# Kernel optimization log

Measured on AMD Instinct MI355X. Metric: run time of the kernel, lower is better.

The kernel has to match this reference:

```python
import jax, jax.numpy as jnp
import numpy as np

B, T, IN, D = 32, 1024, 1536, 768


def setup_inputs() -> dict:
    key = jax.random.key(0)
    ks = jax.random.split(key, 14)
    s_in = 1.0 / np.sqrt(IN)
    s_d = 1.0 / np.sqrt(D)
    return {
        "x": jax.random.normal(ks[0], (B, T, IN), jnp.float32),
        # fc1/fc2 torch Linear weights stored [out, in]
        "fc1_w": jax.random.normal(ks[1], (IN, IN), jnp.float32) * s_in,
        "fc1_b": jax.random.normal(ks[2], (IN,), jnp.float32) * 0.01,
        "fc2_w": jax.random.normal(ks[3], (D, IN), jnp.float32) * s_in,
        "fc2_b": jax.random.normal(ks[4], (D,), jnp.float32) * 0.01,
        # Unary: Conv1d(D,D,k=1) then Conv1d(D,1,k=1); k=1 conv == per-token linear
        "un_emb_w": jax.random.normal(ks[5], (D, D), jnp.float32) * s_d,
        "un_emb_b": jax.random.normal(ks[6], (D,), jnp.float32) * 0.01,
        "un_red_w": jax.random.normal(ks[7], (1, D), jnp.float32) * s_d,
        "un_red_b": jax.random.normal(ks[8], (1,), jnp.float32) * 0.01,
        # Self Pairwise: x_embedding / y_embedding Conv1d(D,D,k=1)
        "pw_x_w": jax.random.normal(ks[9], (D, D), jnp.float32) * s_d,
        "pw_x_b": jax.random.normal(ks[10], (D,), jnp.float32) * 0.01,
        "pw_y_w": jax.random.normal(ks[11], (D, D), jnp.float32) * s_d,
        "pw_y_b": jax.random.normal(ks[12], (D,), jnp.float32) * 0.01,
        # reduce_potentials: Conv1d(2,1,k=1,bias=False) -> 2 scalars
        "red_w": jax.random.normal(ks[13], (2,), jnp.float32),
    }


def reference(x, fc1_w, fc1_b, fc2_w, fc2_b,
              un_emb_w, un_emb_b, un_red_w, un_red_b,
              pw_x_w, pw_x_b, pw_y_w, pw_y_b, red_w):
    # FGAEmbedder MLP: fc2(relu(fc1(x)))
    h = jax.nn.relu(jnp.einsum('bti,oi->bto', x, fc1_w) + fc1_b)
    u = jnp.einsum('bti,oi->bto', h, fc2_w) + fc2_b            # [B,T,D]

    # Unary potential (dropout is identity at inference)
    e = jax.nn.relu(jnp.einsum('btd,od->bto', u, un_emb_w) + un_emb_b)
    un_pot = (jnp.einsum('btd,od->bto', e, un_red_w) + un_red_b)[..., 0]  # [B,T]

    # Self pairwise: cosine-similarity matrix, marginalized by mean (spatial_dim=None)
    xe = jnp.einsum('btd,od->bto', u, pw_x_w) + pw_x_b
    ye = jnp.einsum('btd,od->bto', u, pw_y_w) + pw_y_b
    xn = xe / jnp.maximum(jnp.linalg.norm(xe, axis=-1, keepdims=True), 1e-12)
    yn = ye / jnp.maximum(jnp.linalg.norm(ye, axis=-1, keepdims=True), 1e-12)
    S = jnp.einsum('btd,bsd->bts', xn, yn)                     # [B,T,T]
    pw_pot = jnp.mean(S, axis=2)                               # [B,T]

    # reduce potentials (Conv1d 2->1 no bias; order: unary then self), softmax attention
    scores = red_w[0] * un_pot + red_w[1] * pw_pot             # [B,T]
    w = jax.nn.softmax(scores, axis=1)
    return jnp.einsum('btd,bt->bd', u, w)                      # [B,D]
```

## Files before the change

kernel.cpp:

```cpp
#include <hip/hip_runtime.h>
#include <stdint.h>

#define MROWS 32768
#define TSEQ  1024
#define BBATCH 32
#define INDIM 1536
#define DDIM  768
#define NCAT  2304

typedef short short8 __attribute__((ext_vector_type(8)));
typedef short short4v __attribute__((ext_vector_type(4)));
typedef float f32x4  __attribute__((ext_vector_type(4)));

__device__ __forceinline__ float b2f(ushort u) {
    union { uint32_t u; float f; } x; x.u = ((uint32_t)u) << 16; return x.f;
}
__device__ __forceinline__ ushort f2b(float f) {
    union { float f; uint32_t u; } x; x.f = f;
    uint32_t r = x.u + 0x7fffu + ((x.u >> 16) & 1u);
    return (ushort)(r >> 16);
}

__global__ void cvt_bf16(const float* __restrict__ in, ushort* __restrict__ out, int n4) {
    int i = blockIdx.x * blockDim.x + threadIdx.x;
    if (i < n4) {
        float4 v = ((const float4*)in)[i];
        ushort4 o;
        o.x = f2b(v.x); o.y = f2b(v.y); o.z = f2b(v.z); o.w = f2b(v.w);
        ((ushort4*)out)[i] = o;
    }
}

__device__ __forceinline__ void cvt4(const float* __restrict__ in, ushort* __restrict__ out, int i) {
    float4 v = ((const float4*)in)[i];
    ushort4 o;
    o.x = f2b(v.x); o.y = f2b(v.y); o.z = f2b(v.z); o.w = f2b(v.w);
    ((ushort4*)out)[i] = o;
}

__global__ void cvt_weights(const float* __restrict__ fc1_w, const float* __restrict__ fc2_w,
                            const float* __restrict__ w3a, const float* __restrict__ w3b,
                            const float* __restrict__ w3c,
                            const float* __restrict__ ba, const float* __restrict__ bb,
                            const float* __restrict__ bc,
                            ushort* __restrict__ W1, ushort* __restrict__ W2,
                            ushort* __restrict__ W3, float* __restrict__ B3,
                            float* __restrict__ ybar_zero, float* __restrict__ out_zero)
{
    int i = blockIdx.x * 256 + threadIdx.x;
    if (i < 589824)        cvt4(fc1_w, W1, i);
    else if (i < 884736)   cvt4(fc2_w, W2, i - 589824);
    else if (i < 1032192)  cvt4(w3a,  W3,           i - 884736);
    else if (i < 1179648)  cvt4(w3b,  W3 + 589824,  i - 1032192);
    else if (i < 1327104)  cvt4(w3c,  W3 + 1179648, i - 1179648);
    else if (i < 1327680) {
        int j = i - 1327104;
        const float* src = (j < 192) ? ba : (j < 384) ? bb : bc;
        int off = (j < 192) ? j : (j < 384) ? (j - 192) : (j - 384);
        ((float4*)B3)[j] = ((const float4*)src)[off];
    }
    else if (i < 1333824) {
        float4 z = {0.f, 0.f, 0.f, 0.f};
        ((float4*)ybar_zero)[i - 1327680] = z;
    }
    else if (i < 1339968) {
        float4 z = {0.f, 0.f, 0.f, 0.f};
        ((float4*)out_zero)[i - 1333824] = z;
    }
}

__global__ __launch_bounds__(256, 2)
void gemm_bt(const ushort* __restrict__ A, const ushort* __restrict__ Bm,
             const float* __restrict__ bias, ushort* __restrict__ C,
             int M, int N, int K, int relu_ncols)
{
    __shared__ __align__(16) ushort lA[128 * 64];
    __shared__ __align__(16) ushort lB[128 * 64];

    const int tid  = threadIdx.x;
    const int lane = tid & 63, wave = tid >> 6;
    const int wm = wave & 1, wn = wave >> 1;
    const int quad = lane >> 4, r16 = lane & 15;

    const int ntiles = N >> 7;
    const int xcd = blockIdx.x & 7;
    const int j   = blockIdx.x >> 3;
    const int g   = j / ntiles;
    const int n_t = j - g * ntiles;
    const int m_t = xcd + (g << 3);
    const int m0 = m_t * 128, n0 = n_t * 128;

    const int srow = lane >> 2;
    const int scol = ((lane & 3) ^ ((lane >> 3) & 3)) * 8;
    const int goff = (r16 << 5) + ((quad ^ ((r16 >> 1) & 3)) << 3);

    f32x4 acc[4][4] = {};

    const int kIters = K >> 6;
    for (int kt = 0; kt < kIters; ++kt) {
        const int k0 = kt << 6;
        __syncthreads();
#pragma unroll
        for (int c = 0; c < 4; ++c) {
            int S  = wave * 4 + c;
            int kh = S >> 3, rs = S & 7;
            int row = rs * 16 + srow;
            int kc  = k0 + kh * 32 + scol;
            const ushort* ga = A + (size_t)(m0 + row) * K + kc;
            __builtin_amdgcn_global_load_lds(
                (const __attribute__((address_space(1))) void*)ga,
                (__attribute__((address_space(3))) void*)&lA[S * 512], 16, 0, 0);
            const ushort* gb = Bm + (size_t)(n0 + row) * K + kc;
            __builtin_amdgcn_global_load_lds(
                (const __attribute__((address_space(1))) void*)gb,
                (__attribute__((address_space(3))) void*)&lB[S * 512], 16, 0, 0);
        }
        __syncthreads();

#pragma unroll
        for (int kh = 0; kh < 2; ++kh) {
            short8 af[4], bf[4];
#pragma unroll
            for (int i = 0; i < 4; ++i)
                af[i] = *(const short8*)&lA[kh * 4096 + (wm * 4 + i) * 512 + goff];
#pragma unroll
            for (int j2 = 0; j2 < 4; ++j2)
                bf[j2] = *(const short8*)&lB[kh * 4096 + (wn * 4 + j2) * 512 + goff];
#pragma unroll
            for (int i = 0; i < 4; ++i)
#pragma unroll
                for (int j2 = 0; j2 < 4; ++j2)
                    acc[i][j2] = __builtin_amdgcn_mfma_f32_16x16x32_bf16(af[i], bf[j2], acc[i][j2], 0, 0, 0);
        }
    }

#pragma unroll
    for (int j2 = 0; j2 < 4; ++j2) {
        int gn = n0 + wn * 64 + j2 * 16 + r16;
        float bv = bias[gn];
        bool dorelu = gn < relu_ncols;
#pragma unroll
        for (int i = 0; i < 4; ++i) {
            int gmb = m0 + wm * 64 + i * 16 + quad * 4;
#pragma unroll
            for (int rr = 0; rr < 4; ++rr) {
                float v = acc[i][j2][rr] + bv;
                if (dorelu) v = fmaxf(v, 0.f);
                C[(size_t)(gmb + rr) * N + gn] = f2b(v);
            }
        }
    }
}

__global__ void row_stats_k(const ushort* __restrict__ G3, const float* __restrict__ urw,
                            float* __restrict__ se_o, float* __restrict__ sx_o,
                            float* __restrict__ sy_o)
{
    int m = blockIdx.x, tid = threadIdx.x;
    const ushort* row = G3 + (size_t)m * NCAT;
    float se = 0.f, sx = 0.f, sy = 0.f;
    for (int c = tid; c < 288; c += 256) {
        short8 v = *(const short8*)(row + c * 8);
        if (c < 96) {
            const float4 u0 = ((const float4*)urw)[c * 2];
            const float4 u1 = ((const float4*)urw)[c * 2 + 1];
            se += b2f((ushort)v[0]) * u0.x + b2f((ushort)v[1]) * u0.y
                + b2f((ushort)v[2]) * u0.z + b2f((ushort)v[3]) * u0.w
                + b2f((ushort)v[4]) * u1.x + b2f((ushort)v[5]) * u1.y
                + b2f((ushort)v[6]) * u1.z + b2f((ushort)v[7]) * u1.w;
        } else {
            float a = 0.f;
#pragma unroll
            for (int k = 0; k < 8; ++k) { float f = b2f((ushort)v[k]); a += f * f; }
            if (c < 192) sx += a; else sy += a;
        }
    }
    for (int off = 32; off; off >>= 1) {
        se += __shfl_down(se, off, 64);
        sx += __shfl_down(sx, off, 64);
        sy += __shfl_down(sy, off, 64);
    }
    __shared__ float rb[3][4];
    int lane = tid & 63, w = tid >> 6;
    if (lane == 0) { rb[0][w] = se; rb[1][w] = sx; rb[2][w] = sy; }
    __syncthreads();
    if (tid == 0) {
        se_o[m] = rb[0][0] + rb[0][1] + rb[0][2] + rb[0][3];
        sx_o[m] = rb[1][0] + rb[1][1] + rb[1][2] + rb[1][3];
        sy_o[m] = rb[2][0] + rb[2][1] + rb[2][2] + rb[2][3];
    }
}

__global__ void ybar_k(const ushort* __restrict__ G3, const float* __restrict__ sy,
                       float* __restrict__ ybar)
{
    int b = blockIdx.x, s0 = blockIdx.y * 32;
    int tid = threadIdx.x;
    __shared__ float sr[32];
    if (tid < 32) {
        float v = sy[b * TSEQ + s0 + tid];
        sr[tid] = (1.0f / TSEQ) / fmaxf(sqrtf(v), 1e-12f);
    }
    __syncthreads();
    float a0 = 0.f, a1 = 0.f, a2 = 0.f;
#pragma unroll 8
    for (int s = 0; s < 32; ++s) {
        const ushort* row = G3 + (size_t)(b * TSEQ + s0 + s) * NCAT + 2 * DDIM;
        float w = sr[s];
        a0 += b2f(row[tid])       * w;
        a1 += b2f(row[tid + 256]) * w;
        a2 += b2f(row[tid + 512]) * w;
    }
    atomicAdd(&ybar[b * DDIM + tid],       a0);
    atomicAdd(&ybar[b * DDIM + tid + 256], a1);
    atomicAdd(&ybar[b * DDIM + tid + 512], a2);
}

__global__ void pw_scores_k(const ushort* __restrict__ G3, const float* __restrict__ ybar,
                            const float* __restrict__ se_i, const float* __restrict__ sx_i,
                            const float* __restrict__ urb, const float* __restrict__ red_w,
                            float* __restrict__ scores)
{
    int m = blockIdx.x, tid = threadIdx.x;
    int b = m >> 10;
    float s = 0.f;
    if (tid < 192) {
        short4v v = *(const short4v*)(G3 + (size_t)m * NCAT + DDIM + tid * 4);
        float4 yv = ((const float4*)(ybar + b * DDIM))[tid];
        s = b2f((ushort)v[0]) * yv.x + b2f((ushort)v[1]) * yv.y
          + b2f((ushort)v[2]) * yv.z + b2f((ushort)v[3]) * yv.w;
    }
    for (int off = 32; off; off >>= 1) s += __shfl_down(s, off, 64);
    __shared__ float rb[4];
    int lane = tid & 63, w = tid >> 6;
    if (lane == 0) rb[w] = s;
    __syncthreads();
    if (tid == 0) {
        float dot = rb[0] + rb[1] + rb[2] + rb[3];
        float rnx = 1.f / fmaxf(sqrtf(sx_i[m]), 1e-12f);
        float un_pot = se_i[m] + urb[0];
        scores[m] = red_w[0] * un_pot + red_w[1] * (rnx * dot);
    }
}

__global__ void softmax_k(const float* __restrict__ scores, float* __restrict__ wsm)
{
    int b = blockIdx.x, tid = threadIdx.x;
    float v[4];
    float lm = -1e30f;
#pragma unroll
    for (int i = 0; i < 4; ++i) {
        v[i] = scores[b * TSEQ + i * 256 + tid];
        lm = fmaxf(lm, v[i]);
    }
    for (int off = 32; off; off >>= 1) lm = fmaxf(lm, __shfl_down(lm, off, 64));
    __shared__ float rb[4];
    __shared__ float smax, ssum;
    int lane = tid & 63, w = tid >> 6;
    if (lane == 0) rb[w] = lm;
    __syncthreads();
    if (tid == 0) smax = fmaxf(fmaxf(rb[0], rb[1]), fmaxf(rb[2], rb[3]));
    __syncthreads();
    float e[4];
    float ls = 0.f;
#pragma unroll
    for (int i = 0; i < 4; ++i) { e[i] = expf(v[i] - smax); ls += e[i]; }
    for (int off = 32; off; off >>= 1) ls += __shfl_down(ls, off, 64);
    __syncthreads();
    if (lane == 0) rb[w] = ls;
    __syncthreads();
    if (tid == 0) ssum = rb[0] + rb[1] + rb[2] + rb[3];
    __syncthreads();
    float inv = 1.f / ssum;
#pragma unroll
    for (int i = 0; i < 4; ++i) wsm[b * TSEQ + i * 256 + tid] = e[i] * inv;
}

__global__ void out_k(const ushort* __restrict__ U16, const float* __restrict__ wsm,
                      float* __restrict__ out)
{
    int b = blockIdx.x, t0 = blockIdx.y * 32;
    int tid = threadIdx.x;
    __shared__ float sw[32];
    if (tid < 32) sw[tid] = wsm[b * TSEQ + t0 + tid];
    __syncthreads();
    float a0 = 0.f, a1 = 0.f, a2 = 0.f;
#pragma unroll 8
    for (int t = 0; t < 32; ++t) {
        const ushort* row = U16 + (size_t)(b * TSEQ + t0 + t) * DDIM;
        float w = sw[t];
        a0 += b2f(row[tid])       * w;
        a1 += b2f(row[tid + 256]) * w;
        a2 += b2f(row[tid + 512]) * w;
    }
    atomicAdd(&out[b * DDIM + tid],       a0);
    atomicAdd(&out[b * DDIM + tid + 256], a1);
    atomicAdd(&out[b * DDIM + tid + 512], a2);
}

static const size_t O_X16   = 0;
static const size_t O_H16   = 100663296;
static const size_t O_G3    = 0;
static const size_t O_U16   = 201326592;
static const size_t O_W1    = 251658240;
static const size_t O_W2    = 256376832;
static const size_t O_W3    = 258736128;
static const size_t O_B3    = 262275072;
static const size_t O_SE    = 262284288;
static const size_t O_SX    = 262415360;
static const size_t O_SY    = 262546432;
static const size_t O_SCORE = 262677504;
static const size_t O_WSM   = 262808576;
static const size_t O_YBAR  = 262939648;

extern "C" void kernel_launch(void* const* d_in, const int* in_sizes, int n_in,
                              void* d_out, int out_size, void* d_ws, size_t ws_size,
                              hipStream_t stream)
{
    const float* x        = (const float*)d_in[0];
    const float* fc1_w    = (const float*)d_in[1];
    const float* fc1_b    = (const float*)d_in[2];
    const float* fc2_w    = (const float*)d_in[3];
    const float* fc2_b    = (const float*)d_in[4];
    const float* un_emb_w = (const float*)d_in[5];
    const float* un_emb_b = (const float*)d_in[6];
    const float* un_red_w = (const float*)d_in[7];
    const float* un_red_b = (const float*)d_in[8];
    const float* pw_x_w   = (const float*)d_in[9];
    const float* pw_x_b   = (const float*)d_in[10];
    const float* pw_y_w   = (const float*)d_in[11];
    const float* pw_y_b   = (const float*)d_in[12];
    const float* red_w    = (const float*)d_in[13];

    char* ws = (char*)d_ws;
    ushort* X16 = (ushort*)(ws + O_X16);
    ushort* H16 = (ushort*)(ws + O_H16);
    ushort* G3  = (ushort*)(ws + O_G3);
    ushort* U16 = (ushort*)(ws + O_U16);
    ushort* W1  = (ushort*)(ws + O_W1);
    ushort* W2  = (ushort*)(ws + O_W2);
    ushort* W3  = (ushort*)(ws + O_W3);
    float*  B3  = (float*)(ws + O_B3);
    float*  SE  = (float*)(ws + O_SE);
    float*  SX  = (float*)(ws + O_SX);
    float*  SY  = (float*)(ws + O_SY);
    float*  SCORES = (float*)(ws + O_SCORE);
    float*  WSM = (float*)(ws + O_WSM);
    float*  YBAR = (float*)(ws + O_YBAR);

    cvt_bf16<<<49152, 256, 0, stream>>>(x, X16, 12582912);
    cvt_weights<<<5235, 256, 0, stream>>>(fc1_w, fc2_w, un_emb_w, pw_x_w, pw_y_w,
                                          un_emb_b, pw_x_b, pw_y_b, W1, W2, W3, B3,
                                          YBAR, (float*)d_out);

    gemm_bt<<<(MROWS / 128) * (INDIM / 128), 256, 0, stream>>>(
        X16, W1, fc1_b, H16, MROWS, INDIM, INDIM, INDIM);
    gemm_bt<<<(MROWS / 128) * (DDIM / 128), 256, 0, stream>>>(
        H16, W2, fc2_b, U16, MROWS, DDIM, INDIM, 0);
    gemm_bt<<<(MROWS / 128) * (NCAT / 128), 256, 0, stream>>>(
        U16, W3, B3, G3, MROWS, NCAT, DDIM, DDIM);

    row_stats_k<<<MROWS, 256, 0, stream>>>(G3, un_red_w, SE, SX, SY);
    ybar_k<<<dim3(BBATCH, 32), 256, 0, stream>>>(G3, SY, YBAR);
    pw_scores_k<<<MROWS, 256, 0, stream>>>(G3, YBAR, SE, SX, un_red_b, red_w, SCORES);
    softmax_k<<<BBATCH, 256, 0, stream>>>(SCORES, WSM);
    out_k<<<dim3(BBATCH, 32), 256, 0, stream>>>(U16, WSM, (float*)d_out);
}
```

Before: 754.0 us.

## Fuse row stats into GEMM epilogue and merge tail kernels cooperatively

Merges the input and weight conversion kernels into one launch. The per-row unary dot product and squared norms are now computed in the third GEMM's epilogue with a shuffle reduction and atomics, which removes the separate row_stats pass that re-read the large G3 buffer. The ybar, score, softmax and weighted-output kernels are merged into one cooperative kernel with grid syncs, which cuts launch overhead. In exchange, the stats are accumulated in fp32 before bf16 rounding, and the GEMM epilogue gains extra atomics.

```diff
diff --git a/kernel.cpp b/kernel.cpp
--- a/kernel.cpp
+++ b/kernel.cpp
@@ -1,5 +1,8 @@
 #include <hip/hip_runtime.h>
+#include <hip/hip_cooperative_groups.h>
 #include <stdint.h>
+
+namespace cg = cooperative_groups;
 
 #define MROWS 32768
 #define TSEQ  1024
@@ -21,16 +24,6 @@
     return (ushort)(r >> 16);
 }
 
-__global__ void cvt_bf16(const float* __restrict__ in, ushort* __restrict__ out, int n4) {
-    int i = blockIdx.x * blockDim.x + threadIdx.x;
-    if (i < n4) {
-        float4 v = ((const float4*)in)[i];
-        ushort4 o;
-        o.x = f2b(v.x); o.y = f2b(v.y); o.z = f2b(v.z); o.w = f2b(v.w);
-        ((ushort4*)out)[i] = o;
-    }
-}
-
 __device__ __forceinline__ void cvt4(const float* __restrict__ in, ushort* __restrict__ out, int i) {
     float4 v = ((const float4*)in)[i];
     ushort4 o;
@@ -38,41 +31,52 @@
     ((ushort4*)out)[i] = o;
 }
 
-__global__ void cvt_weights(const float* __restrict__ fc1_w, const float* __restrict__ fc2_w,
-                            const float* __restrict__ w3a, const float* __restrict__ w3b,
-                            const float* __restrict__ w3c,
-                            const float* __restrict__ ba, const float* __restrict__ bb,
-                            const float* __restrict__ bc,
-                            ushort* __restrict__ W1, ushort* __restrict__ W2,
-                            ushort* __restrict__ W3, float* __restrict__ B3,
-                            float* __restrict__ ybar_zero, float* __restrict__ out_zero)
+#define C0 12582912
+#define C1 13172736
+#define C2 13467648
+#define C3 13615104
+#define C4 13762560
+#define C5 13910016
+#define C6 13910592
+#define C7 13916736
+#define C8 13922880
+#define C9 13947456
+__global__ void cvt_all(const float* __restrict__ x,
+                        const float* __restrict__ fc1_w, const float* __restrict__ fc2_w,
+                        const float* __restrict__ w3a, const float* __restrict__ w3b,
+                        const float* __restrict__ w3c,
+                        const float* __restrict__ ba, const float* __restrict__ bb,
+                        const float* __restrict__ bc,
+                        ushort* __restrict__ X16, ushort* __restrict__ W1,
+                        ushort* __restrict__ W2, ushort* __restrict__ W3,
+                        float* __restrict__ B3, float* __restrict__ ybar_z,
+                        float* __restrict__ out_z, float* __restrict__ stats_z)
 {
     int i = blockIdx.x * 256 + threadIdx.x;
-    if (i < 589824)        cvt4(fc1_w, W1, i);
-    else if (i < 884736)   cvt4(fc2_w, W2, i - 589824);
-    else if (i < 1032192)  cvt4(w3a,  W3,           i - 884736);
-    else if (i < 1179648)  cvt4(w3b,  W3 + 589824,  i - 1032192);
-    else if (i < 1327104)  cvt4(w3c,  W3 + 1179648, i - 1179648);
-    else if (i < 1327680) {
-        int j = i - 1327104;
+    float4 z = {0.f, 0.f, 0.f, 0.f};
+    if (i < C0)       cvt4(x, X16, i);
+    else if (i < C1)  cvt4(fc1_w, W1, i - C0);
+    else if (i < C2)  cvt4(fc2_w, W2, i - C1);
+    else if (i < C3)  cvt4(w3a, W3,           i - C2);
+    else if (i < C4)  cvt4(w3b, W3 + 589824,  i - C3);
+    else if (i < C5)  cvt4(w3c, W3 + 1179648, i - C4);
+    else if (i < C6) {
+        int j = i - C5;
         const float* src = (j < 192) ? ba : (j < 384) ? bb : bc;
         int off = (j < 192) ? j : (j < 384) ? (j - 192) : (j - 384);
         ((float4*)B3)[j] = ((const float4*)src)[off];
     }
-    else if (i < 1333824) {
-        float4 z = {0.f, 0.f, 0.f, 0.f};
-        ((float4*)ybar_zero)[i - 1327680] = z;
-    }
-    else if (i < 1339968) {
-        float4 z = {0.f, 0.f, 0.f, 0.f};
-        ((float4*)out_zero)[i - 1333824] = z;
-    }
+    else if (i < C7)  ((float4*)ybar_z)[i - C6] = z;
+    else if (i < C8)  ((float4*)out_z)[i - C7] = z;
+    else if (i < C9)  ((float4*)stats_z)[i - C8] = z;
 }
 
 __global__ __launch_bounds__(256, 2)
 void gemm_bt(const ushort* __restrict__ A, const ushort* __restrict__ Bm,
              const float* __restrict__ bias, ushort* __restrict__ C,
-             int M, int N, int K, int relu_ncols)
+             int M, int N, int K, int relu_ncols,
+             const float* __restrict__ urw, float* __restrict__ SE,
+             float* __restrict__ SX, float* __restrict__ SY)
 {
     __shared__ __align__(16) ushort lA[128 * 64];
     __shared__ __align__(16) ushort lB[128 * 64];
@@ -134,11 +138,15 @@
         }
     }
 
+    const bool stats = (urw != nullptr);
+    const int sec = n0 / DDIM;
+    float st[4][4] = {};
 #pragma unroll
     for (int j2 = 0; j2 < 4; ++j2) {
         int gn = n0 + wn * 64 + j2 * 16 + r16;
         float bv = bias[gn];
         bool dorelu = gn < relu_ncols;
+        float uw = (stats && sec == 0) ? urw[gn] : 0.f;
 #pragma unroll
         for (int i = 0; i < 4; ++i) {
             int gmb = m0 + wm * 64 + i * 16 + quad * 4;
@@ -147,155 +155,141 @@
                 float v = acc[i][j2][rr] + bv;
                 if (dorelu) v = fmaxf(v, 0.f);
                 C[(size_t)(gmb + rr) * N + gn] = f2b(v);
+                if (stats) st[i][rr] += (sec == 0) ? v * uw : v * v;
             }
         }
     }
-}
-
-__global__ void row_stats_k(const ushort* __restrict__ G3, const float* __restrict__ urw,
-                            float* __restrict__ se_o, float* __restrict__ sx_o,
-                            float* __restrict__ sy_o)
+    if (stats) {
+#pragma unroll
+        for (int i = 0; i < 4; ++i)
+#pragma unroll
+            for (int rr = 0; rr < 4; ++rr) {
+                float v = st[i][rr];
+                v += __shfl_xor(v, 1, 64);
+                v += __shfl_xor(v, 2, 64);
+                v += __shfl_xor(v, 4, 64);
+                v += __shfl_xor(v, 8, 64);
+                st[i][rr] = v;
+            }
+        if (r16 == 0) {
+            float* dst = (sec == 0) ? SE : (sec == 1) ? SX : SY;
+#pragma unroll
+            for (int i = 0; i < 4; ++i)
+#pragma unroll
+                for (int rr = 0; rr < 4; ++rr)
+                    atomicAdd(&dst[m0 + wm * 64 + i * 16 + quad * 4 + rr], st[i][rr]);
+        }
+    }
+}
+
+__global__ __launch_bounds__(256, 4)
+void tail_coop(const ushort* __restrict__ G3, const ushort* __restrict__ U16,
+               const float* __restrict__ SE, const float* __restrict__ SX,
+               const float* __restrict__ SY, const float* __restrict__ urb,
+               const float* __restrict__ red_w, float* __restrict__ ybar,
+               float* __restrict__ scores, float* __restrict__ wsm,
+               float* __restrict__ out)
 {
-    int m = blockIdx.x, tid = threadIdx.x;
-    const ushort* row = G3 + (size_t)m * NCAT;
-    float se = 0.f, sx = 0.f, sy = 0.f;
-    for (int c = tid; c < 288; c += 256) {
-        short8 v = *(const short8*)(row + c * 8);
-        if (c < 96) {
-            const float4 u0 = ((const float4*)urw)[c * 2];
-            const float4 u1 = ((const float4*)urw)[c * 2 + 1];
-            se += b2f((ushort)v[0]) * u0.x + b2f((ushort)v[1]) * u0.y
-                + b2f((ushort)v[2]) * u0.z + b2f((ushort)v[3]) * u0.w
-                + b2f((ushort)v[4]) * u1.x + b2f((ushort)v[5]) * u1.y
-                + b2f((ushort)v[6]) * u1.z + b2f((ushort)v[7]) * u1.w;
-        } else {
-            float a = 0.f;
-#pragma unroll
-            for (int k = 0; k < 8; ++k) { float f = b2f((ushort)v[k]); a += f * f; }
-            if (c < 192) sx += a; else sy += a;
-        }
-    }
-    for (int off = 32; off; off >>= 1) {
-        se += __shfl_down(se, off, 64);
-        sx += __shfl_down(sx, off, 64);
-        sy += __shfl_down(sy, off, 64);
-    }
-    __shared__ float rb[3][4];
-    int lane = tid & 63, w = tid >> 6;
-    if (lane == 0) { rb[0][w] = se; rb[1][w] = sx; rb[2][w] = sy; }
-    __syncthreads();
-    if (tid == 0) {
-        se_o[m] = rb[0][0] + rb[0][1] + rb[0][2] + rb[0][3];
-        sx_o[m] = rb[1][0] + rb[1][1] + rb[1][2] + rb[1][3];
-        sy_o[m] = rb[2][0] + rb[2][1] + rb[2][2] + rb[2][3];
-    }
-}
-
-__global__ void ybar_k(const ushort* __restrict__ G3, const float* __restrict__ sy,
-                       float* __restrict__ ybar)
-{
-    int b = blockIdx.x, s0 = blockIdx.y * 32;
-    int tid = threadIdx.x;
-    __shared__ float sr[32];
-    if (tid < 32) {
-        float v = sy[b * TSEQ + s0 + tid];
-        sr[tid] = (1.0f / TSEQ) / fmaxf(sqrtf(v), 1e-12f);
-    }
-    __syncthreads();
-    float a0 = 0.f, a1 = 0.f, a2 = 0.f;
+    cg::grid_group grid = cg::this_grid();
+    const int tid = threadIdx.x;
+    const int lane = tid & 63, wv = tid >> 6;
+    __shared__ float smem[64];
+
+    {
+        int b = blockIdx.x >> 5, s0 = (blockIdx.x & 31) * 32;
+        if (tid < 32) {
+            float v = SY[b * TSEQ + s0 + tid];
+            smem[tid] = (1.0f / TSEQ) / fmaxf(sqrtf(v), 1e-12f);
+        }
+        __syncthreads();
+        float a0 = 0.f, a1 = 0.f, a2 = 0.f;
 #pragma unroll 8
-    for (int s = 0; s < 32; ++s) {
-        const ushort* row = G3 + (size_t)(b * TSEQ + s0 + s) * NCAT + 2 * DDIM;
-        float w = sr[s];
-        a0 += b2f(row[tid])       * w;
-        a1 += b2f(row[tid + 256]) * w;
-        a2 += b2f(row[tid + 512]) * w;
-    }
-    atomicAdd(&ybar[b * DDIM + tid],       a0);
-    atomicAdd(&ybar[b * DDIM + tid + 256], a1);
-    atomicAdd(&ybar[b * DDIM + tid + 512], a2);
-}
-
-__global__ void pw_scores_k(const ushort* __restrict__ G3, const float* __restrict__ ybar,
-                            const float* __restrict__ se_i, const float* __restrict__ sx_i,
-                            const float* __restrict__ urb, const float* __restrict__ red_w,
-                            float* __restrict__ scores)
-{
-    int m = blockIdx.x, tid = threadIdx.x;
-    int b = m >> 10;
-    float s = 0.f;
-    if (tid < 192) {
-        short4v v = *(const short4v*)(G3 + (size_t)m * NCAT + DDIM + tid * 4);
-        float4 yv = ((const float4*)(ybar + b * DDIM))[tid];
-        s = b2f((ushort)v[0]) * yv.x + b2f((ushort)v[1]) * yv.y
-          + b2f((ushort)v[2]) * yv.z + b2f((ushort)v[3]) * yv.w;
-    }
-    for (int off = 32; off; off >>= 1) s += __shfl_down(s, off, 64);
-    __shared__ float rb[4];
-    int lane = tid & 63, w = tid >> 6;
-    if (lane == 0) rb[w] = s;
-    __syncthreads();
-    if (tid == 0) {
-        float dot = rb[0] + rb[1] + rb[2] + rb[3];
-        float rnx = 1.f / fmaxf(sqrtf(sx_i[m]), 1e-12f);
-        float un_pot = se_i[m] + urb[0];
-        scores[m] = red_w[0] * un_pot + red_w[1] * (rnx * dot);
-    }
-}
-
-__global__ void softmax_k(const float* __restrict__ scores, float* __restrict__ wsm)
-{
-    int b = blockIdx.x, tid = threadIdx.x;
-    float v[4];
-    float lm = -1e30f;
-#pragma unroll
-    for (int i = 0; i < 4; ++i) {
-        v[i] = scores[b * TSEQ + i * 256 + tid];
-        lm = fmaxf(lm, v[i]);
-    }
-    for (int off = 32; off; off >>= 1) lm = fmaxf(lm, __shfl_down(lm, off, 64));
-    __shared__ float rb[4];
-    __shared__ float smax, ssum;
-    int lane = tid & 63, w = tid >> 6;
-    if (lane == 0) rb[w] = lm;
-    __syncthreads();
-    if (tid == 0) smax = fmaxf(fmaxf(rb[0], rb[1]), fmaxf(rb[2], rb[3]));
-    __syncthreads();
-    float e[4];
-    float ls = 0.f;
-#pragma unroll
-    for (int i = 0; i < 4; ++i) { e[i] = expf(v[i] - smax); ls += e[i]; }
-    for (int off = 32; off; off >>= 1) ls += __shfl_down(ls, off, 64);
-    __syncthreads();
-    if (lane == 0) rb[w] = ls;
-    __syncthreads();
-    if (tid == 0) ssum = rb[0] + rb[1] + rb[2] + rb[3];
-    __syncthreads();
-    float inv = 1.f / ssum;
-#pragma unroll
-    for (int i = 0; i < 4; ++i) wsm[b * TSEQ + i * 256 + tid] = e[i] * inv;
-}
-
-__global__ void out_k(const ushort* __restrict__ U16, const float* __restrict__ wsm,
-                      float* __restrict__ out)
-{
-    int b = blockIdx.x, t0 = blockIdx.y * 32;
-    int tid = threadIdx.x;
-    __shared__ float sw[32];
-    if (tid < 32) sw[tid] = wsm[b * TSEQ + t0 + tid];
-    __syncthreads();
-    float a0 = 0.f, a1 = 0.f, a2 = 0.f;
+        for (int s = 0; s < 32; ++s) {
+            const ushort* row = G3 + (size_t)(b * TSEQ + s0 + s) * NCAT + 2 * DDIM;
+            float w = smem[s];
+            a0 += b2f(row[tid])       * w;
+            a1 += b2f(row[tid + 256]) * w;
+            a2 += b2f(row[tid + 512]) * w;
+        }
+        atomicAdd(&ybar[b * DDIM + tid],       a0);
+        atomicAdd(&ybar[b * DDIM + tid + 256], a1);
+        atomicAdd(&ybar[b * DDIM + tid + 512], a2);
+    }
+    __threadfence();
+    grid.sync();
+
+    {
+        for (int k = 0; k < 8; ++k) {
+            int m = blockIdx.x * 32 + wv * 8 + k;
+            int b = m >> 10;
+            const ushort* xe = G3 + (size_t)m * NCAT + DDIM;
+            const float4* yb = (const float4*)(ybar + b * DDIM);
+            float s = 0.f;
+#pragma unroll
+            for (int c0 = 0; c0 < 3; ++c0) {
+                int c = lane + c0 * 64;
+                short4v v = *(const short4v*)(xe + c * 4);
+                float4 yv = yb[c];
+                s += b2f((ushort)v[0]) * yv.x + b2f((ushort)v[1]) * yv.y
+                   + b2f((ushort)v[2]) * yv.z + b2f((ushort)v[3]) * yv.w;
+            }
+#pragma unroll
+            for (int off = 32; off; off >>= 1) s += __shfl_xor(s, off, 64);
+            if (lane == 0) {
+                float rnx = 1.f / fmaxf(sqrtf(SX[m]), 1e-12f);
+                scores[m] = red_w[0] * (SE[m] + urb[0]) + red_w[1] * (rnx * s);
+            }
+        }
+    }
+    __threadfence();
+    grid.sync();
+
+    if (blockIdx.x < BBATCH) {
+        int b = blockIdx.x;
+        float v[4];
+        float lm = -1e30f;
+#pragma unroll
+        for (int i = 0; i < 4; ++i) {
+            v[i] = scores[b * TSEQ + i * 256 + tid];
+            lm = fmaxf(lm, v[i]);
+        }
+        for (int off = 32; off; off >>= 1) lm = fmaxf(lm, __shfl_down(lm, off, 64));
+        if (lane == 0) smem[wv] = lm;
+        __syncthreads();
+        float smax = fmaxf(fmaxf(smem[0], smem[1]), fmaxf(smem[2], smem[3]));
+        float e[4];
+        float ls = 0.f;
+#pragma unroll
+        for (int i = 0; i < 4; ++i) { e[i] = expf(v[i] - smax); ls += e[i]; }
+        for (int off = 32; off; off >>= 1) ls += __shfl_down(ls, off, 64);
+        __syncthreads();
+        if (lane == 0) smem[8 + wv] = ls;
+        __syncthreads();
+        float inv = 1.f / (smem[8] + smem[9] + smem[10] + smem[11]);
+#pragma unroll
+        for (int i = 0; i < 4; ++i) wsm[b * TSEQ + i * 256 + tid] = e[i] * inv;
+    }
+    __threadfence();
+    grid.sync();
+
+    {
+        int b = blockIdx.x >> 5, t0 = (blockIdx.x & 31) * 32;
+        __syncthreads();
+        if (tid < 32) smem[tid] = wsm[b * TSEQ + t0 + tid];
+        __syncthreads();
+        float a0 = 0.f, a1 = 0.f, a2 = 0.f;
 #pragma unroll 8
-    for (int t = 0; t < 32; ++t) {
-        const ushort* row = U16 + (size_t)(b * TSEQ + t0 + t) * DDIM;
-        float w = sw[t];
-        a0 += b2f(row[tid])       * w;
-        a1 += b2f(row[tid + 256]) * w;
-        a2 += b2f(row[tid + 512]) * w;
-    }
-    atomicAdd(&out[b * DDIM + tid],       a0);
-    atomicAdd(&out[b * DDIM + tid + 256], a1);
-    atomicAdd(&out[b * DDIM + tid + 512], a2);
+        for (int t = 0; t < 32; ++t) {
+            const ushort* row = U16 + (size_t)(b * TSEQ + t0 + t) * DDIM;
+            float w = smem[t];
+            a0 += b2f(row[tid])       * w;
+            a1 += b2f(row[tid + 256]) * w;
+            a2 += b2f(row[tid + 512]) * w;
+        }
+        atomicAdd(&out[b * DDIM + tid],       a0);
+        atomicAdd(&out[b * DDIM + tid + 256], a1);
+        atomicAdd(&out[b * DDIM + tid + 512], a2);
+    }
 }
 
 static const size_t O_X16   = 0;
@@ -348,21 +342,22 @@
     float*  WSM = (float*)(ws + O_WSM);
     float*  YBAR = (float*)(ws + O_YBAR);
 
-    cvt_bf16<<<49152, 256, 0, stream>>>(x, X16, 12582912);
-    cvt_weights<<<5235, 256, 0, stream>>>(fc1_w, fc2_w, un_emb_w, pw_x_w, pw_y_w,
-                                          un_emb_b, pw_x_b, pw_y_b, W1, W2, W3, B3,
-                                          YBAR, (float*)d_out);
+    cvt_all<<<54483, 256, 0, stream>>>(x, fc1_w, fc2_w, un_emb_w, pw_x_w, pw_y_w,
+                                       un_emb_b, pw_x_b, pw_y_b,
+                                       X16, W1, W2, W3, B3, YBAR, (float*)d_out, SE);
 
     gemm_bt<<<(MROWS / 128) * (INDIM / 128), 256, 0, stream>>>(
-        X16, W1, fc1_b, H16, MROWS, INDIM, INDIM, INDIM);
+        X16, W1, fc1_b, H16, MROWS, INDIM, INDIM, INDIM,
+        nullptr, nullptr, nullptr, nullptr);
     gemm_bt<<<(MROWS / 128) * (DDIM / 128), 256, 0, stream>>>(
-        H16, W2, fc2_b, U16, MROWS, DDIM, INDIM, 0);
+        H16, W2, fc2_b, U16, MROWS, DDIM, INDIM, 0,
+        nullptr, nullptr, nullptr, nullptr);
     gemm_bt<<<(MROWS / 128) * (NCAT / 128), 256, 0, stream>>>(
-        U16, W3, B3, G3, MROWS, NCAT, DDIM, DDIM);
-
-    row_stats_k<<<MROWS, 256, 0, stream>>>(G3, un_red_w, SE, SX, SY);
-    ybar_k<<<dim3(BBATCH, 32), 256, 0, stream>>>(G3, SY, YBAR);
-    pw_scores_k<<<MROWS, 256, 0, stream>>>(G3, YBAR, SE, SX, un_red_b, red_w, SCORES);
-    softmax_k<<<BBATCH, 256, 0, stream>>>(SCORES, WSM);
-    out_k<<<dim3(BBATCH, 32), 256, 0, stream>>>(U16, WSM, (float*)d_out);
-}
+        U16, W3, B3, G3, MROWS, NCAT, DDIM, DDIM,
+        un_red_w, SE, SX, SY);
+
+    void* args[] = { (void*)&G3, (void*)&U16, (void*)&SE, (void*)&SX, (void*)&SY,
+                     (void*)&un_red_b, (void*)&red_w, (void*)&YBAR, (void*)&SCORES,
+                     (void*)&WSM, (void*)&d_out };
+    hipLaunchCooperativeKernel((void*)tail_coop, dim3(1024), dim3(256), args, 0, stream);
+}
```

Result: slower. 1.258 ms (+66.8%).
